# Kernel optimization log

Measured on AMD Instinct MI355X. Metric: run time of the kernel, lower is better.

## Reference

```python
import jax, jax.numpy as jnp
import numpy as np

B, S, D, H = 4, 2048, 1024, 16
HD = D // H


def setup_inputs() -> dict:
    key = jax.random.key(0)
    ks = jax.random.split(key, 10)
    x = jax.random.normal(ks[0], (B, S, D), dtype=jnp.float32)
    mask = jnp.zeros((B, 1, 1, S), dtype=jnp.float32)  # 1 = masked, 0 = keep
    sc = 1.0 / np.sqrt(D)
    wq = jax.random.normal(ks[1], (D, D), dtype=jnp.float32) * sc
    wk = jax.random.normal(ks[2], (D, D), dtype=jnp.float32) * sc
    wv = jax.random.normal(ks[3], (D, D), dtype=jnp.float32) * sc
    wo = jax.random.normal(ks[4], (D, D), dtype=jnp.float32) * sc
    bq = jnp.zeros((D,), jnp.float32)
    bk = jnp.zeros((D,), jnp.float32)
    bv = jnp.zeros((D,), jnp.float32)
    bo = jnp.zeros((D,), jnp.float32)
    return {"x": x, "mask": mask, "wq": wq, "bq": bq, "wk": wk, "bk": bk,
            "wv": wv, "bv": bv, "wo": wo, "bo": bo}


def _split_heads(t):
    # (B, S, D) -> (B, H, S, HD)
    return t.reshape(B, -1, H, HD).transpose(0, 2, 1, 3)


def reference(x, mask, wq, bq, wk, bk, wv, bv, wo, bo):
    q = _split_heads(x @ wq + bq)
    k = _split_heads(x @ wk + bk)
    v = _split_heads(x @ wv + bv)
    # scaled dot-product attention (TF tutorial convention: mask*-1e9 added)
    scores = jnp.einsum("bhqd,bhkd->bhqk", q, k) / jnp.sqrt(jnp.float32(HD))
    scores = scores + mask * -1e9
    attn_weights = jax.nn.softmax(scores, axis=-1)  # (B, H, Sq, Sk)
    attn = jnp.einsum("bhqk,bhkd->bhqd", attn_weights, v)
    attn = attn.transpose(0, 2, 1, 3).reshape(B, -1, D)
    out = attn @ wo + bo
    return out, attn_weights
```

## Files before the change

kernel.cpp:

```cpp
#include <hip/hip_runtime.h>
#include <hip/hip_bf16.h>

#define S_LEN  2048
#define DMODEL 1024
#define NHEAD  16
#define HDIM   64
#define BSZ    4

#define C_SCORE  0.18033688f
#define C_MASK  -1.4426950e9f

typedef __bf16 bf16_t;
typedef __bf16 bf16x8 __attribute__((ext_vector_type(8)));
typedef __bf16 bf16x4 __attribute__((ext_vector_type(4)));
typedef float  f32x4  __attribute__((ext_vector_type(4)));

typedef __attribute__((address_space(1))) void as1_void;
typedef __attribute__((address_space(3))) void as3_void;

__device__ __forceinline__ f32x4 mfma16(bf16x8 a, bf16x8 b, f32x4 c) {
    return __builtin_amdgcn_mfma_f32_16x16x32_bf16(a, b, c, 0, 0, 0);
}

__global__ __launch_bounds__(256) void cvt_x_kernel(const float* __restrict__ x,
                                                    bf16_t* __restrict__ xb, int n4) {
    int i = blockIdx.x * 256 + threadIdx.x;
    int stride = gridDim.x * 256;
    for (; i < n4; i += stride) {
        float4 v = ((const float4*)x)[i];
        bf16x4 t = { (bf16_t)v.x, (bf16_t)v.y, (bf16_t)v.z, (bf16_t)v.w };
        ((bf16x4*)xb)[i] = t;
    }
}

__global__ __launch_bounds__(256) void cvt_wT_kernel(const float* __restrict__ w,
                                                     bf16_t* __restrict__ wT) {
    __shared__ bf16_t t[64][65];
    const int bx = blockIdx.x * 64;
    const int by = blockIdx.y * 64;
    const int tx = threadIdx.x & 63, ty = threadIdx.x >> 6;
    #pragma unroll
    for (int rr = 0; rr < 64; rr += 4)
        t[tx][rr + ty] = (bf16_t)w[(size_t)(bx + rr + ty) * DMODEL + by + tx];
    __syncthreads();
    #pragma unroll
    for (int rr = 0; rr < 64; rr += 4)
        wT[(size_t)(by + rr + ty) * DMODEL + bx + tx] = t[rr + ty][tx];
}

__global__ __launch_bounds__(256) void transpose_v(const bf16_t* __restrict__ V,
                                                   bf16_t* __restrict__ Vt) {
    __shared__ __attribute__((aligned(16))) bf16_t t[64][72];
    const int bh = blockIdx.y;
    const int s0 = blockIdx.x * 64;
    const int tid = threadIdx.x;
    const bf16_t* Vb = V + (size_t)bh * S_LEN * HDIM;
    bf16_t* Vo = Vt + (size_t)bh * HDIM * S_LEN;
    #pragma unroll
    for (int p = 0; p < 2; ++p) {
        const int sl = p * 32 + (tid >> 3);
        const int c8 = (tid & 7) * 8;
        bf16x8 v = *(const bf16x8*)(Vb + (size_t)(s0 + sl) * HDIM + c8);
        #pragma unroll
        for (int j = 0; j < 8; ++j) t[c8 + j][sl] = v[j];
    }
    __syncthreads();
    #pragma unroll
    for (int p = 0; p < 2; ++p) {
        const int dl = p * 32 + (tid >> 3);
        const int s8 = (tid & 7) * 8;
        bf16x8 v = *(const bf16x8*)(&t[dl][s8]);
        *(bf16x8*)(Vo + (size_t)dl * S_LEN + s0 + s8) = v;
    }
}

template <int MODE>
__global__ __launch_bounds__(256) void gemm_bt(const bf16_t* __restrict__ A,
                                               const bf16_t* __restrict__ Bt,
                                               const float* __restrict__ b0,
                                               const float* __restrict__ b1,
                                               const float* __restrict__ b2,
                                               bf16_t* __restrict__ o0,
                                               bf16_t* __restrict__ o1,
                                               bf16_t* __restrict__ o2,
                                               float* __restrict__ of) {
    constexpr int GK = 1024;
    __shared__ __attribute__((aligned(16))) bf16_t As[128 * 32];
    __shared__ __attribute__((aligned(16))) bf16_t Bs[128 * 32];

    const int tid  = threadIdx.x;
    const int wave = tid >> 6, lane = tid & 63;
    const int col16 = lane & 15, g = lane >> 4;
    const int wr = wave >> 1, wc = wave & 1;
    const int bn0 = blockIdx.x * 128, bm0 = blockIdx.y * 128;

    const int r4 = tid >> 2;
    const int c8 = (tid & 3) * 8;

    f32x4 acc[4][4] = {};

    for (int k0 = 0; k0 < GK; k0 += 32) {
        __syncthreads();
        #pragma unroll
        for (int i = 0; i < 2; ++i) {
            __builtin_amdgcn_global_load_lds(
                (const as1_void*)(A + (size_t)(bm0 + i * 64 + r4) * GK + k0 + c8),
                (as3_void*)(As + (i * 64 + wave * 16) * 32), 16, 0, 0);
            __builtin_amdgcn_global_load_lds(
                (const as1_void*)(Bt + (size_t)(bn0 + i * 64 + r4) * GK + k0 + c8),
                (as3_void*)(Bs + (i * 64 + wave * 16) * 32), 16, 0, 0);
        }
        __syncthreads();

        bf16x8 af[4], bfr[4];
        #pragma unroll
        for (int i = 0; i < 4; ++i) {
            af[i]  = *(const bf16x8*)(As + (wr * 64 + i * 16 + col16) * 32 + g * 8);
            bfr[i] = *(const bf16x8*)(Bs + (wc * 64 + i * 16 + col16) * 32 + g * 8);
        }
        #pragma unroll
        for (int mi = 0; mi < 4; ++mi)
            #pragma unroll
            for (int ni = 0; ni < 4; ++ni)
                acc[mi][ni] = mfma16(af[mi], bfr[ni], acc[mi][ni]);
    }

    #pragma unroll
    for (int ni = 0; ni < 4; ++ni) {
        const int gn = bn0 + wc * 64 + ni * 16 + col16;
        if (MODE == 0) {
            const int proj = bn0 >> 10;
            const float* bias = proj == 0 ? b0 : (proj == 1 ? b1 : b2);
            bf16_t* outp      = proj == 0 ? o0 : (proj == 1 ? o1 : o2);
            const int n1 = gn & 1023, h = n1 >> 6, hd = n1 & 63;
            const float bv = bias[n1];
            #pragma unroll
            for (int mi = 0; mi < 4; ++mi)
                #pragma unroll
                for (int r = 0; r < 4; ++r) {
                    const int gm = bm0 + wr * 64 + mi * 16 + g * 4 + r;
                    const int b = gm >> 11, s = gm & 2047;
                    outp[(((size_t)b * NHEAD + h) * S_LEN + s) * HDIM + hd] =
                        (bf16_t)(acc[mi][ni][r] + bv);
                }
        } else {
            const float bv = b0[gn];
            #pragma unroll
            for (int mi = 0; mi < 4; ++mi)
                #pragma unroll
                for (int r = 0; r < 4; ++r) {
                    const int gm = bm0 + wr * 64 + mi * 16 + g * 4 + r;
                    of[(size_t)gm * DMODEL + gn] = acc[mi][ni][r] + bv;
                }
        }
    }
}

__global__ __launch_bounds__(256, 2) void attn_fused(const bf16_t* __restrict__ Q,
                                                     const bf16_t* __restrict__ K,
                                                     const bf16_t* __restrict__ Vt,
                                                     const float* __restrict__ mask,
                                                     float* __restrict__ attnW,
                                                     bf16_t* __restrict__ ctx) {
    __shared__ __attribute__((aligned(16))) bf16_t Ks[2][64][64];
    __shared__ __attribute__((aligned(16))) bf16_t Vs[2][64][64];
    __shared__ __attribute__((aligned(16))) float  Pl[4][32][64];
    __shared__ __attribute__((aligned(16))) float  Ml[S_LEN];

    const int tid = threadIdx.x, wave = tid >> 6, lane = tid & 63;
    const int col16 = lane & 15, g = lane >> 4;
    const int r7 = col16 & 7;

    const int lin = blockIdx.x;
    const int logical = (lin & 7) * 64 + (lin >> 3);
    const int bh = logical >> 3, pp = logical & 7;
    const int b = bh >> 4, h = bh & 15;
    const int qA = pp * 256 + wave * 32;
    const int qB = pp * 256 + 128 + wave * 32;

    const bf16_t* Qb = Q + (size_t)bh * S_LEN * HDIM;
    const bf16_t* Kb = K + (size_t)bh * S_LEN * HDIM;
    const bf16_t* Vb = Vt + (size_t)bh * HDIM * S_LEN;
    const float* mp = mask + (size_t)b * S_LEN;

    #pragma unroll
    for (int i = 0; i < 2; ++i) {
        const int idx = i * 256 + tid;
        f32x4 v = ((const f32x4*)mp)[idx];
        #pragma unroll
        for (int r = 0; r < 4; ++r) v[r] *= C_MASK;
        *(f32x4*)(&Ml[idx * 4]) = v;
    }

    const int srow  = lane >> 3;
    const int sunit = (lane & 7) ^ srow;

    auto stageK = [&](int buf, int it) {
        const int kk0 = it << 6;
        #pragma unroll
        for (int i2 = 0; i2 < 2; ++i2) {
            const int i = wave * 2 + i2;
            __builtin_amdgcn_global_load_lds(
                (const as1_void*)(Kb + (size_t)(kk0 + i * 8 + srow) * HDIM + sunit * 8),
                (as3_void*)(&Ks[buf][i * 8][0]), 16, 0, 0);
        }
    };
    auto stageV = [&](int buf, int it) {
        const int kk0 = it << 6;
        #pragma unroll
        for (int i2 = 0; i2 < 2; ++i2) {
            const int i = wave * 2 + i2;
            __builtin_amdgcn_global_load_lds(
                (const as1_void*)(Vb + (size_t)(i * 8 + srow) * S_LEN + kk0 + sunit * 8),
                (as3_void*)(&Vs[buf][i * 8][0]), 16, 0, 0);
        }
    };
    auto kfrag = [&](int buf, int nj, int kh) {
        return *(const bf16x8*)(&Ks[buf][nj * 16 + col16][(((kh * 4 + g) ^ r7) * 8)]);
    };
    auto vfrag = [&](int buf, int nd, int kh) {
        return *(const bf16x8*)(&Vs[buf][nd * 16 + col16][(((kh * 4 + g) ^ r7) * 8)]);
    };

    bf16x8 qa0[2][2], qa1[2][2];
    #pragma unroll
    for (int hh = 0; hh < 2; ++hh)
        #pragma unroll
        for (int kh = 0; kh < 2; ++kh) {
            qa0[hh][kh] = *(const bf16x8*)(Qb + (size_t)(qA + hh * 16 + col16) * HDIM +
                                           kh * 32 + g * 8);
            qa1[hh][kh] = *(const bf16x8*)(Qb + (size_t)(qB + hh * 16 + col16) * HDIM +
                                           kh * 32 + g * 8);
        }

    f32x4 lacc[2] = {};
    stageK(0, 0);
    __syncthreads();

    for (int it = 0; it < 32; ++it) {
        const int kk0 = it << 6, cur = it & 1;
        if (it < 31) stageK(cur ^ 1, it + 1);
        f32x4 mvr[4];
        #pragma unroll
        for (int nj = 0; nj < 4; ++nj)
            mvr[nj] = *(const f32x4*)(&Ml[kk0 + nj * 16 + g * 4]);
        #pragma unroll
        for (int nj = 0; nj < 4; ++nj) {
            const bf16x8 kf0 = kfrag(cur, nj, 0);
            const bf16x8 kf1 = kfrag(cur, nj, 1);
            f32x4 t0 = {0.f, 0.f, 0.f, 0.f}, t1 = {0.f, 0.f, 0.f, 0.f};
            t0 = mfma16(kf0, qa0[0][0], t0);
            t0 = mfma16(kf1, qa0[0][1], t0);
            t1 = mfma16(kf0, qa0[1][0], t1);
            t1 = mfma16(kf1, qa0[1][1], t1);
            #pragma unroll
            for (int r = 0; r < 4; ++r) {
                lacc[0][r] += exp2f(fmaf(t0[r], C_SCORE, mvr[nj][r]));
                lacc[1][r] += exp2f(fmaf(t1[r], C_SCORE, mvr[nj][r]));
            }
        }
        asm volatile("s_waitcnt vmcnt(0)" ::: "memory");
        __builtin_amdgcn_sched_barrier(0);
        __builtin_amdgcn_s_barrier();
    }

    float crow0[2];
    #pragma unroll
    for (int hh = 0; hh < 2; ++hh) {
        float lr = (lacc[hh][0] + lacc[hh][1]) + (lacc[hh][2] + lacc[hh][3]);
        lr += __shfl_xor(lr, 16);
        lr += __shfl_xor(lr, 32);
        crow0[hh] = -__log2f(lr);
        lacc[hh] = (f32x4){0.f, 0.f, 0.f, 0.f};
    }

    f32x4 o[2][4] = {};
    float* awbase = attnW + ((size_t)bh * S_LEN + qA) * S_LEN;

    stageK(0, 0);
    stageV(0, 0);
    asm volatile("s_waitcnt vmcnt(0)" ::: "memory");
    __builtin_amdgcn_sched_barrier(0);
    __builtin_amdgcn_s_barrier();

    for (int it = 0; it < 32; ++it) {
        const int kk0 = it << 6, cur = it & 1;
        if (it < 31) { stageK(cur ^ 1, it + 1); stageV(cur ^ 1, it + 1); }
        f32x4 mvr[4];
        #pragma unroll
        for (int nj = 0; nj < 4; ++nj)
            mvr[nj] = *(const f32x4*)(&Ml[kk0 + nj * 16 + g * 4]);

        #pragma unroll
        for (int nj = 0; nj < 4; ++nj) {
            const bf16x8 kf0 = kfrag(cur, nj, 0);
            const bf16x8 kf1 = kfrag(cur, nj, 1);
            f32x4 s0 = {0.f, 0.f, 0.f, 0.f}, s1 = {0.f, 0.f, 0.f, 0.f};
            f32x4 u0 = {0.f, 0.f, 0.f, 0.f}, u1 = {0.f, 0.f, 0.f, 0.f};
            s0 = mfma16(kf0, qa0[0][0], s0);
            s0 = mfma16(kf1, qa0[0][1], s0);
            s1 = mfma16(kf0, qa0[1][0], s1);
            s1 = mfma16(kf1, qa0[1][1], s1);
            u0 = mfma16(kf0, qa1[0][0], u0);
            u0 = mfma16(kf1, qa1[0][1], u0);
            u1 = mfma16(kf0, qa1[1][0], u1);
            u1 = mfma16(kf1, qa1[1][1], u1);
            f32x4 pn0, pn1;
            #pragma unroll
            for (int r = 0; r < 4; ++r) {
                const float mm = mvr[nj][r];
                pn0[r] = exp2f(fmaf(s0[r], C_SCORE, mm + crow0[0]));
                pn1[r] = exp2f(fmaf(s1[r], C_SCORE, mm + crow0[1]));
                lacc[0][r] += exp2f(fmaf(u0[r], C_SCORE, mm));
                lacc[1][r] += exp2f(fmaf(u1[r], C_SCORE, mm));
            }
            const int pw = ((nj * 4 + g) ^ r7) * 4;
            *(f32x4*)(&Pl[wave][col16][pw])      = pn0;
            *(f32x4*)(&Pl[wave][16 + col16][pw]) = pn1;
        }

        #pragma unroll
        for (int j = 0; j < 8; ++j) {
            const int row = j * 4 + (lane >> 4);
            const int u = lane & 15;
            const f32x4 v = *(const f32x4*)(&Pl[wave][row][((u ^ (row & 7)) * 4)]);
            __builtin_nontemporal_store(v, (f32x4*)(awbase + (size_t)row * S_LEN + kk0 + u * 4));
        }

        #pragma unroll
        for (int hh = 0; hh < 2; ++hh)
            #pragma unroll
            for (int kh = 0; kh < 2; ++kh) {
                const int u0i = kh * 8 + g * 2;
                const f32x4 a0 = *(const f32x4*)(&Pl[wave][hh * 16 + col16][((u0i ^ r7) * 4)]);
                const f32x4 a1 = *(const f32x4*)(&Pl[wave][hh * 16 + col16][(((u0i + 1) ^ r7) * 4)]);
                bf16x8 pa;
                #pragma unroll
                for (int j = 0; j < 4; ++j) {
                    pa[j]     = (bf16_t)a0[j];
                    pa[4 + j] = (bf16_t)a1[j];
                }
                #pragma unroll
                for (int nd = 0; nd < 4; ++nd)
                    o[hh][nd] = mfma16(vfrag(cur, nd, kh), pa, o[hh][nd]);
            }

        asm volatile("s_waitcnt vmcnt(8)" ::: "memory");
        __builtin_amdgcn_sched_barrier(0);
        __builtin_amdgcn_s_barrier();
    }

    float crow1[2];
    #pragma unroll
    for (int hh = 0; hh < 2; ++hh) {
        float lr = (lacc[hh][0] + lacc[hh][1]) + (lacc[hh][2] + lacc[hh][3]);
        lr += __shfl_xor(lr, 16);
        lr += __shfl_xor(lr, 32);
        crow1[hh] = -__log2f(lr);
    }

    #pragma unroll
    for (int hh = 0; hh < 2; ++hh) {
        bf16_t* cp = ctx + ((size_t)b * S_LEN + qA + hh * 16 + col16) * DMODEL + h * HDIM;
        #pragma unroll
        for (int nd = 0; nd < 4; ++nd) {
            bf16x4 cv;
            #pragma unroll
            for (int r = 0; r < 4; ++r) cv[r] = (bf16_t)o[hh][nd][r];
            *(bf16x4*)(cp + nd * 16 + g * 4) = cv;
        }
        o[hh][0] = o[hh][1] = o[hh][2] = o[hh][3] = (f32x4){0.f, 0.f, 0.f, 0.f};
    }

    awbase = attnW + ((size_t)bh * S_LEN + qB) * S_LEN;

    stageK(0, 0);
    stageV(0, 0);
    asm volatile("s_waitcnt vmcnt(0)" ::: "memory");
    __builtin_amdgcn_sched_barrier(0);
    __builtin_amdgcn_s_barrier();

    for (int it = 0; it < 32; ++it) {
        const int kk0 = it << 6, cur = it & 1;
        if (it < 31) { stageK(cur ^ 1, it + 1); stageV(cur ^ 1, it + 1); }
        f32x4 mvr[4];
        #pragma unroll
        for (int nj = 0; nj < 4; ++nj)
            mvr[nj] = *(const f32x4*)(&Ml[kk0 + nj * 16 + g * 4]);

        #pragma unroll
        for (int nj = 0; nj < 4; ++nj) {
            const bf16x8 kf0 = kfrag(cur, nj, 0);
            const bf16x8 kf1 = kfrag(cur, nj, 1);
            f32x4 t0 = {0.f, 0.f, 0.f, 0.f}, t1 = {0.f, 0.f, 0.f, 0.f};
            t0 = mfma16(kf0, qa1[0][0], t0);
            t0 = mfma16(kf1, qa1[0][1], t0);
            t1 = mfma16(kf0, qa1[1][0], t1);
            t1 = mfma16(kf1, qa1[1][1], t1);
            f32x4 pn0, pn1;
            #pragma unroll
            for (int r = 0; r < 4; ++r) {
                const float mm = mvr[nj][r];
                pn0[r] = exp2f(fmaf(t0[r], C_SCORE, mm + crow1[0]));
                pn1[r] = exp2f(fmaf(t1[r], C_SCORE, mm + crow1[1]));
            }
            const int pw = ((nj * 4 + g) ^ r7) * 4;
            *(f32x4*)(&Pl[wave][col16][pw])      = pn0;
            *(f32x4*)(&Pl[wave][16 + col16][pw]) = pn1;
        }

        #pragma unroll
        for (int j = 0; j < 8; ++j) {
            const int row = j * 4 + (lane >> 4);
            const int u = lane & 15;
            const f32x4 v = *(const f32x4*)(&Pl[wave][row][((u ^ (row & 7)) * 4)]);
            __builtin_nontemporal_store(v, (f32x4*)(awbase + (size_t)row * S_LEN + kk0 + u * 4));
        }

        #pragma unroll
        for (int hh = 0; hh < 2; ++hh)
            #pragma unroll
            for (int kh = 0; kh < 2; ++kh) {
                const int u0i = kh * 8 + g * 2;
                const f32x4 a0 = *(const f32x4*)(&Pl[wave][hh * 16 + col16][((u0i ^ r7) * 4)]);
                const f32x4 a1 = *(const f32x4*)(&Pl[wave][hh * 16 + col16][(((u0i + 1) ^ r7) * 4)]);
                bf16x8 pa;
                #pragma unroll
                for (int j = 0; j < 4; ++j) {
                    pa[j]     = (bf16_t)a0[j];
                    pa[4 + j] = (bf16_t)a1[j];
                }
                #pragma unroll
                for (int nd = 0; nd < 4; ++nd)
                    o[hh][nd] = mfma16(vfrag(cur, nd, kh), pa, o[hh][nd]);
            }

        asm volatile("s_waitcnt vmcnt(8)" ::: "memory");
        __builtin_amdgcn_sched_barrier(0);
        __builtin_amdgcn_s_barrier();
    }

    #pragma unroll
    for (int hh = 0; hh < 2; ++hh) {
        bf16_t* cp = ctx + ((size_t)b * S_LEN + qB + hh * 16 + col16) * DMODEL + h * HDIM;
        #pragma unroll
        for (int nd = 0; nd < 4; ++nd) {
            bf16x4 cv;
            #pragma unroll
            for (int r = 0; r < 4; ++r) cv[r] = (bf16_t)o[hh][nd][r];
            *(bf16x4*)(cp + nd * 16 + g * 4) = cv;
        }
    }
}

extern "C" void kernel_launch(void* const* d_in, const int* in_sizes, int n_in,
                              void* d_out, int out_size, void* d_ws, size_t ws_size,
                              hipStream_t stream) {
    const float* x    = (const float*)d_in[0];
    const float* mask = (const float*)d_in[1];
    const float* wq   = (const float*)d_in[2];
    const float* bq   = (const float*)d_in[3];
    const float* wk   = (const float*)d_in[4];
    const float* bk   = (const float*)d_in[5];
    const float* wv   = (const float*)d_in[6];
    const float* bv   = (const float*)d_in[7];
    const float* wo   = (const float*)d_in[8];
    const float* bo   = (const float*)d_in[9];

    const size_t nX = (size_t)BSZ * S_LEN * DMODEL;
    const size_t nW = (size_t)DMODEL * DMODEL;

    char* ws = (char*)d_ws;
    size_t off = 0;
    bf16_t* xb     = (bf16_t*)(ws + off); off += nX * 2;
    bf16_t* wqkvT  = (bf16_t*)(ws + off); off += 3 * nW * 2;
    bf16_t* woT    = (bf16_t*)(ws + off); off += nW * 2;
    bf16_t* qbh    = (bf16_t*)(ws + off); off += nX * 2;
    bf16_t* kbh    = (bf16_t*)(ws + off); off += nX * 2;
    bf16_t* vrow   = (bf16_t*)(ws + off); off += nX * 2;
    bf16_t* vtb    = (bf16_t*)(ws + off); off += nX * 2;
    bf16_t* ctx    = (bf16_t*)(ws + off); off += nX * 2;
    if (ws_size < off) return;

    float* outp  = (float*)d_out;
    float* attnW = outp + nX;

    cvt_x_kernel<<<4096, 256, 0, stream>>>(x, xb, (int)(nX / 4));
    cvt_wT_kernel<<<dim3(16, 16), 256, 0, stream>>>(wq, wqkvT);
    cvt_wT_kernel<<<dim3(16, 16), 256, 0, stream>>>(wk, wqkvT + nW);
    cvt_wT_kernel<<<dim3(16, 16), 256, 0, stream>>>(wv, wqkvT + 2 * nW);
    cvt_wT_kernel<<<dim3(16, 16), 256, 0, stream>>>(wo, woT);

    gemm_bt<0><<<dim3(24, 64), 256, 0, stream>>>(xb, wqkvT, bq, bk, bv,
                                                 qbh, kbh, vrow, nullptr);
    transpose_v<<<dim3(32, 64), 256, 0, stream>>>(vrow, vtb);

    attn_fused<<<512, 256, 0, stream>>>(qbh, kbh, vtb, mask, attnW, ctx);

    gemm_bt<2><<<dim3(8, 64), 256, 0, stream>>>(ctx, woT, bo, nullptr, nullptr,
                                                nullptr, nullptr, nullptr, outp);
}
```

Before: 382.7 us.

## Fuse conversion kernels, write V transposed from QKV GEMM, widen K tile

Merges the x conversion and the four weight-transpose kernels into one launch. The QKV GEMM now writes the V projection directly in transposed per-head layout through an LDS staging buffer, which removes the separate transpose kernel and its round trip through global memory. The attention kernel's first pass (row-sum) stages 128 keys per iteration instead of 64, halving its loop trips and barriers. In exchange the GEMM and attention kernels use larger shared-memory footprints, and woT relies on being contiguous after wqkvT.

```diff
diff --git a/kernel.cpp b/kernel.cpp
--- a/kernel.cpp
+++ b/kernel.cpp
@@ -22,22 +22,32 @@
     return __builtin_amdgcn_mfma_f32_16x16x32_bf16(a, b, c, 0, 0, 0);
 }
 
-__global__ __launch_bounds__(256) void cvt_x_kernel(const float* __restrict__ x,
-                                                    bf16_t* __restrict__ xb, int n4) {
-    int i = blockIdx.x * 256 + threadIdx.x;
-    int stride = gridDim.x * 256;
-    for (; i < n4; i += stride) {
-        float4 v = ((const float4*)x)[i];
-        bf16x4 t = { (bf16_t)v.x, (bf16_t)v.y, (bf16_t)v.z, (bf16_t)v.w };
-        ((bf16x4*)xb)[i] = t;
-    }
-}
-
-__global__ __launch_bounds__(256) void cvt_wT_kernel(const float* __restrict__ w,
-                                                     bf16_t* __restrict__ wT) {
+__global__ __launch_bounds__(256) void cvt_all(const float* __restrict__ x,
+                                               bf16_t* __restrict__ xb,
+                                               const float* __restrict__ w0,
+                                               const float* __restrict__ w1,
+                                               const float* __restrict__ w2,
+                                               const float* __restrict__ w3,
+                                               bf16_t* __restrict__ wT) {
     __shared__ bf16_t t[64][65];
-    const int bx = blockIdx.x * 64;
-    const int by = blockIdx.y * 64;
+    const int bid = blockIdx.x;
+    if (bid < 4096) {
+        const int i0 = bid * 256 + threadIdx.x;
+        #pragma unroll
+        for (int rep = 0; rep < 2; ++rep) {
+            const int i = i0 + rep * 1048576;
+            float4 v = ((const float4*)x)[i];
+            bf16x4 tv = { (bf16_t)v.x, (bf16_t)v.y, (bf16_t)v.z, (bf16_t)v.w };
+            ((bf16x4*)xb)[i] = tv;
+        }
+        return;
+    }
+    const int wb = bid - 4096;
+    const int wsel = wb >> 8;
+    const float* w = wsel == 0 ? w0 : (wsel == 1 ? w1 : (wsel == 2 ? w2 : w3));
+    bf16_t* wTo = wT + (size_t)wsel * DMODEL * DMODEL;
+    const int rb = wb & 255;
+    const int bx = (rb & 15) * 64, by = (rb >> 4) * 64;
     const int tx = threadIdx.x & 63, ty = threadIdx.x >> 6;
     #pragma unroll
     for (int rr = 0; rr < 64; rr += 4)
@@ -45,33 +55,7 @@
     __syncthreads();
     #pragma unroll
     for (int rr = 0; rr < 64; rr += 4)
-        wT[(size_t)(by + rr + ty) * DMODEL + bx + tx] = t[rr + ty][tx];
-}
-
-__global__ __launch_bounds__(256) void transpose_v(const bf16_t* __restrict__ V,
-                                                   bf16_t* __restrict__ Vt) {
-    __shared__ __attribute__((aligned(16))) bf16_t t[64][72];
-    const int bh = blockIdx.y;
-    const int s0 = blockIdx.x * 64;
-    const int tid = threadIdx.x;
-    const bf16_t* Vb = V + (size_t)bh * S_LEN * HDIM;
-    bf16_t* Vo = Vt + (size_t)bh * HDIM * S_LEN;
-    #pragma unroll
-    for (int p = 0; p < 2; ++p) {
-        const int sl = p * 32 + (tid >> 3);
-        const int c8 = (tid & 7) * 8;
-        bf16x8 v = *(const bf16x8*)(Vb + (size_t)(s0 + sl) * HDIM + c8);
-        #pragma unroll
-        for (int j = 0; j < 8; ++j) t[c8 + j][sl] = v[j];
-    }
-    __syncthreads();
-    #pragma unroll
-    for (int p = 0; p < 2; ++p) {
-        const int dl = p * 32 + (tid >> 3);
-        const int s8 = (tid & 7) * 8;
-        bf16x8 v = *(const bf16x8*)(&t[dl][s8]);
-        *(bf16x8*)(Vo + (size_t)dl * S_LEN + s0 + s8) = v;
-    }
+        wTo[(size_t)(by + rr + ty) * DMODEL + bx + tx] = t[rr + ty][tx];
 }
 
 template <int MODE>
@@ -85,8 +69,9 @@
                                                bf16_t* __restrict__ o2,
                                                float* __restrict__ of) {
     constexpr int GK = 1024;
-    __shared__ __attribute__((aligned(16))) bf16_t As[128 * 32];
-    __shared__ __attribute__((aligned(16))) bf16_t Bs[128 * 32];
+    __shared__ __attribute__((aligned(16))) bf16_t smem_ab[8704];
+    bf16_t* As = smem_ab;
+    bf16_t* Bs = smem_ab + 4096;
 
     const int tid  = threadIdx.x;
     const int wave = tid >> 6, lane = tid & 63;
@@ -125,13 +110,49 @@
                 acc[mi][ni] = mfma16(af[mi], bfr[ni], acc[mi][ni]);
     }
 
+    if (MODE == 0 && (bn0 >> 10) == 2) {
+        const int n1base = bn0 - 2048;
+        const int brow = bm0 >> 11;
+        const int s0 = bm0 & 2047;
+        __syncthreads();
+        #pragma unroll
+        for (int p = 0; p < 2; ++p) {
+            if (p) __syncthreads();
+            if (wc == p) {
+                #pragma unroll
+                for (int ni = 0; ni < 4; ++ni) {
+                    const float bv = b2[n1base + p * 64 + ni * 16 + col16];
+                    #pragma unroll
+                    for (int mi = 0; mi < 4; ++mi) {
+                        bf16x4 pv;
+                        #pragma unroll
+                        for (int r = 0; r < 4; ++r) pv[r] = (bf16_t)(acc[mi][ni][r] + bv);
+                        *(bf16x4*)&smem_ab[(ni * 16 + col16) * 136 + wr * 64 + mi * 16 + g * 4] = pv;
+                    }
+                }
+            }
+            __syncthreads();
+            const int h2 = (n1base + p * 64) >> 6;
+            bf16_t* vout = o2 + (((size_t)brow * NHEAD + h2) * HDIM) * S_LEN + s0;
+            #pragma unroll
+            for (int j = 0; j < 4; ++j) {
+                const int unit = j * 256 + tid;
+                const int row = unit >> 4;
+                const int cu = (unit & 15) * 8;
+                bf16x8 v = *(const bf16x8*)&smem_ab[row * 136 + cu];
+                *(bf16x8*)(vout + (size_t)row * S_LEN + cu) = v;
+            }
+        }
+        return;
+    }
+
     #pragma unroll
     for (int ni = 0; ni < 4; ++ni) {
         const int gn = bn0 + wc * 64 + ni * 16 + col16;
         if (MODE == 0) {
             const int proj = bn0 >> 10;
-            const float* bias = proj == 0 ? b0 : (proj == 1 ? b1 : b2);
-            bf16_t* outp      = proj == 0 ? o0 : (proj == 1 ? o1 : o2);
+            const float* bias = proj == 0 ? b0 : b1;
+            bf16_t* outp      = proj == 0 ? o0 : o1;
             const int n1 = gn & 1023, h = n1 >> 6, hd = n1 & 63;
             const float bv = bias[n1];
             #pragma unroll
@@ -162,10 +183,12 @@
                                                      const float* __restrict__ mask,
                                                      float* __restrict__ attnW,
                                                      bf16_t* __restrict__ ctx) {
-    __shared__ __attribute__((aligned(16))) bf16_t Ks[2][64][64];
-    __shared__ __attribute__((aligned(16))) bf16_t Vs[2][64][64];
-    __shared__ __attribute__((aligned(16))) float  Pl[4][32][64];
-    __shared__ __attribute__((aligned(16))) float  Ml[S_LEN];
+    __shared__ __attribute__((aligned(16))) char smem[73728];
+    bf16_t (*KsA)[128][64] = (bf16_t(*)[128][64])smem;
+    bf16_t (*Ks)[64][64]   = (bf16_t(*)[64][64])smem;
+    bf16_t (*Vs)[64][64]   = (bf16_t(*)[64][64])(smem + 16384);
+    float  (*Pl)[32][64]   = (float(*)[32][64])(smem + 32768);
+    float*  Ml             = (float*)(smem + 65536);
 
     const int tid = threadIdx.x, wave = tid >> 6, lane = tid & 63;
     const int col16 = lane & 15, g = lane >> 4;
@@ -195,6 +218,16 @@
     const int srow  = lane >> 3;
     const int sunit = (lane & 7) ^ srow;
 
+    auto stageA = [&](int buf, int it) {
+        const int kk0 = it << 7;
+        #pragma unroll
+        for (int i2 = 0; i2 < 4; ++i2) {
+            const int i = wave * 4 + i2;
+            __builtin_amdgcn_global_load_lds(
+                (const as1_void*)(Kb + (size_t)(kk0 + i * 8 + srow) * HDIM + sunit * 8),
+                (as3_void*)(&KsA[buf][i * 8][0]), 16, 0, 0);
+        }
+    };
     auto stageK = [&](int buf, int it) {
         const int kk0 = it << 6;
         #pragma unroll
@@ -234,20 +267,17 @@
         }
 
     f32x4 lacc[2] = {};
-    stageK(0, 0);
+    stageA(0, 0);
     __syncthreads();
 
-    for (int it = 0; it < 32; ++it) {
-        const int kk0 = it << 6, cur = it & 1;
-        if (it < 31) stageK(cur ^ 1, it + 1);
-        f32x4 mvr[4];
-        #pragma unroll
-        for (int nj = 0; nj < 4; ++nj)
-            mvr[nj] = *(const f32x4*)(&Ml[kk0 + nj * 16 + g * 4]);
-        #pragma unroll
-        for (int nj = 0; nj < 4; ++nj) {
-            const bf16x8 kf0 = kfrag(cur, nj, 0);
-            const bf16x8 kf1 = kfrag(cur, nj, 1);
+    for (int it = 0; it < 16; ++it) {
+        const int kk0 = it << 7, cur = it & 1;
+        if (it < 15) stageA(cur ^ 1, it + 1);
+        #pragma unroll
+        for (int nj = 0; nj < 8; ++nj) {
+            const f32x4 mvr = *(const f32x4*)(&Ml[kk0 + nj * 16 + g * 4]);
+            const bf16x8 kf0 = *(const bf16x8*)(&KsA[cur][nj * 16 + col16][((g ^ r7) * 8)]);
+            const bf16x8 kf1 = *(const bf16x8*)(&KsA[cur][nj * 16 + col16][(((4 + g) ^ r7) * 8)]);
             f32x4 t0 = {0.f, 0.f, 0.f, 0.f}, t1 = {0.f, 0.f, 0.f, 0.f};
             t0 = mfma16(kf0, qa0[0][0], t0);
             t0 = mfma16(kf1, qa0[0][1], t0);
@@ -255,8 +285,8 @@
             t1 = mfma16(kf1, qa0[1][1], t1);
             #pragma unroll
             for (int r = 0; r < 4; ++r) {
-                lacc[0][r] += exp2f(fmaf(t0[r], C_SCORE, mvr[nj][r]));
-                lacc[1][r] += exp2f(fmaf(t1[r], C_SCORE, mvr[nj][r]));
+                lacc[0][r] += exp2f(fmaf(t0[r], C_SCORE, mvr[r]));
+                lacc[1][r] += exp2f(fmaf(t1[r], C_SCORE, mvr[r]));
             }
         }
         asm volatile("s_waitcnt vmcnt(0)" ::: "memory");
@@ -477,7 +507,6 @@
     bf16_t* woT    = (bf16_t*)(ws + off); off += nW * 2;
     bf16_t* qbh    = (bf16_t*)(ws + off); off += nX * 2;
     bf16_t* kbh    = (bf16_t*)(ws + off); off += nX * 2;
-    bf16_t* vrow   = (bf16_t*)(ws + off); off += nX * 2;
     bf16_t* vtb    = (bf16_t*)(ws + off); off += nX * 2;
     bf16_t* ctx    = (bf16_t*)(ws + off); off += nX * 2;
     if (ws_size < off) return;
@@ -485,15 +514,10 @@
     float* outp  = (float*)d_out;
     float* attnW = outp + nX;
 
-    cvt_x_kernel<<<4096, 256, 0, stream>>>(x, xb, (int)(nX / 4));
-    cvt_wT_kernel<<<dim3(16, 16), 256, 0, stream>>>(wq, wqkvT);
-    cvt_wT_kernel<<<dim3(16, 16), 256, 0, stream>>>(wk, wqkvT + nW);
-    cvt_wT_kernel<<<dim3(16, 16), 256, 0, stream>>>(wv, wqkvT + 2 * nW);
-    cvt_wT_kernel<<<dim3(16, 16), 256, 0, stream>>>(wo, woT);
+    cvt_all<<<5120, 256, 0, stream>>>(x, xb, wq, wk, wv, wo, wqkvT);
 
     gemm_bt<0><<<dim3(24, 64), 256, 0, stream>>>(xb, wqkvT, bq, bk, bv,
-                                                 qbh, kbh, vrow, nullptr);
-    transpose_v<<<dim3(32, 64), 256, 0, stream>>>(vrow, vtb);
+                                                 qbh, kbh, vtb, nullptr);
 
     attn_fused<<<512, 256, 0, stream>>>(qbh, kbh, vtb, mask, attnW, ctx);
 
```

Measured after the change: 375.9 us. No clear change (-1.8%).
